# Optimization experiments

Hardware: AMD Instinct MI355X
Metric: run time of the kernel (lower is better)

Reference implementation:

```python
import jax, jax.numpy as jnp
import numpy as np


def setup_inputs() -> dict:
    key = jax.random.key(0)
    ks = jax.random.split(key, 5)
    B, G, p, C = 4, 3, 16, 768
    N = p * p
    s = 1.0 / np.sqrt(C)
    return {
        "x": jax.random.normal(ks[0], (B, G, N, C), dtype=jnp.float32),
        "wq": jax.random.normal(ks[1], (C, C), dtype=jnp.float32) * s,
        "w_kv": jax.random.normal(ks[2], (2 * C, C), dtype=jnp.float32) * s,
        "proj_w": jax.random.normal(ks[3], (C, C), dtype=jnp.float32) * s,
        "proj_b": jnp.zeros((C,), dtype=jnp.float32),
    }


def reference(x, wq, w_kv, proj_w, proj_b):
    NUM_HEADS = 12
    B, G, N, C = x.shape  # G == 3 (triplane)
    p = int(round(N ** 0.5))
    H = NUM_HEADS
    D = C // H

    x5 = x.reshape(B, G, p, p, C)

    # Queries: for plane i, tokens in (row a, col b) order; block layout (i, b, n)
    q_x = jnp.transpose(x5, (1, 0, 2, 3, 4)).reshape(G, B, N, C)  # (3,B,N,C)

    # Context per token (a,b) of plane i: row a of plane (i+1)%3  ++  col b of plane (i+2)%3
    rows_src = jnp.stack([x5[:, (i + 1) % G] for i in range(G)], axis=0)  # (3,B,p,p,C)
    cols_src = jnp.stack([x5[:, (i + 2) % G] for i in range(G)], axis=0)  # (3,B,p,p,C)

    # row a broadcast over column index b -> (3,B,a,b,p,C)
    row_ctx = jnp.broadcast_to(rows_src[:, :, :, None, :, :], (G, B, p, p, p, C)).reshape(G, B, N, p, C)
    # column b broadcast over row index a -> (3,B,a,b,p,C)
    cols_t = jnp.transpose(cols_src, (0, 1, 3, 2, 4))  # (3,B,b,r,C)
    col_ctx = jnp.broadcast_to(cols_t[:, :, None, :, :, :], (G, B, p, p, p, C)).reshape(G, B, N, p, C)

    context = jnp.concatenate([row_ctx, col_ctx], axis=3)  # (3,B,N,2p,C)

    # Projections (torch Linear: y = x @ W^T, no bias for q/kv)
    q = (q_x @ wq.T).reshape(G, B, N, H, D)
    kv = context @ w_kv.T  # (3,B,N,2p,2C)
    k = kv[..., :C].reshape(G, B, N, 2 * p, H, D)
    v = kv[..., C:].reshape(G, B, N, 2 * p, H, D)

    scale = 1.0 / np.sqrt(D)
    scores = jnp.einsum("gbnhd,gbnkhd->gbnhk", q, k) * scale
    attn = jax.nn.softmax(scores, axis=-1)
    out = jnp.einsum("gbnhk,gbnkhd->gbnhd", attn, v).reshape(G, B, N, C)

    # Faithful to original: flat (i,b,n) block order reinterpreted as (B,3,N,C)
    out = out.reshape(B, G, N, C)
    out = out @ proj_w.T + proj_b
    return out
```

## Files before the change

### kernel.cpp

```cpp
#include <hip/hip_runtime.h>
#include <hip/hip_bf16.h>

#define Bc 4
#define Gc 3
#define Nc 256
#define Cc_ 768
#define Dc 64
#define Mrows (Bc*Gc*Nc)
#define QKVc (3*Cc_)
#define Koff Cc_
#define Voff (2*Cc_)

typedef _Float16 half_t;
typedef __attribute__((ext_vector_type(8))) _Float16 f16x8;
typedef __attribute__((ext_vector_type(4))) float f32x4;

#define XN   (Mrows*Cc_)
#define WQN  (Cc_*Cc_)
#define WKVN (2*Cc_*Cc_)
#define PWN  (Cc_*Cc_)

__global__ __launch_bounds__(256) void cvt_all(
    const float* __restrict__ x, const float* __restrict__ wq,
    const float* __restrict__ wkv, const float* __restrict__ pw,
    half_t* __restrict__ x16, half_t* __restrict__ wq16,
    half_t* __restrict__ wkv16, half_t* __restrict__ pw16)
{
    const size_t e = ((size_t)blockIdx.x * 256 + threadIdx.x) * 8;
    const float* s; half_t* d;
    if (e < XN)                    { s = x   + e;                     d = x16   + e; }
    else if (e < XN + WQN)         { s = wq  + (e - XN);              d = wq16  + (e - XN); }
    else if (e < XN + WQN + WKVN)  { s = wkv + (e - XN - WQN);        d = wkv16 + (e - XN - WQN); }
    else                           { s = pw  + (e - XN - WQN - WKVN); d = pw16  + (e - XN - WQN - WKVN); }
    const float4 a = *(const float4*)s;
    const float4 b = *(const float4*)(s + 4);
    f16x8 o;
    o[0] = (half_t)a.x; o[1] = (half_t)a.y; o[2] = (half_t)a.z; o[3] = (half_t)a.w;
    o[4] = (half_t)b.x; o[5] = (half_t)b.y; o[6] = (half_t)b.z; o[7] = (half_t)b.w;
    *(f16x8*)d = o;
}

template<typename OutT, bool BIAS>
__global__ __launch_bounds__(256) void gemm16(
    const half_t* __restrict__ A, const half_t* __restrict__ W,
    OutT* __restrict__ C, const float* __restrict__ bias,
    int M, int Nn, int K)
{
    __shared__ __attribute__((aligned(16))) half_t sm[3][2][4][128][8];

    const int tid = threadIdx.x;
    const int w   = tid >> 6;
    const int l   = tid & 63;
    const int wm  = w >> 1;
    const int wn  = w & 1;
    const int m0  = blockIdx.y << 7;
    const int n0  = blockIdx.x << 7;

    f32x4 acc[4][4] = {};

    auto stage = [&](int buf, int k0) {
        #pragma unroll
        for (int i = 0; i < 2; ++i) {
            const int c   = w * 2 + i;
            const int kg  = c >> 1;
            const int r0  = (c & 1) * 64;
            const half_t* ga = A + (size_t)(m0 + r0 + l) * K + k0 + kg * 8;
            const half_t* gb = W + (size_t)(n0 + r0 + l) * K + k0 + kg * 8;
            __builtin_amdgcn_global_load_lds(
                (__attribute__((address_space(1))) void*)ga,
                (__attribute__((address_space(3))) void*)&sm[buf][0][kg][r0][0],
                16, 0, 0);
            __builtin_amdgcn_global_load_lds(
                (__attribute__((address_space(1))) void*)gb,
                (__attribute__((address_space(3))) void*)&sm[buf][1][kg][r0][0],
                16, 0, 0);
        }
    };

    const int NT = K >> 5;
    stage(0, 0);
    stage(1, 32);

    const int kg = l >> 4;
    const int lr = l & 15;
    int cur = 0;

    for (int t = 0; t < NT; ++t) {
        if (t + 1 < NT) asm volatile("s_waitcnt vmcnt(4)" ::: "memory");
        else            asm volatile("s_waitcnt vmcnt(0)" ::: "memory");
        __builtin_amdgcn_s_barrier();
        if (t + 2 < NT) {
            int nb = cur + 2; if (nb >= 3) nb -= 3;
            stage(nb, (t + 2) << 5);
        }

        f16x8 af[4], bf[4];
        #pragma unroll
        for (int mi = 0; mi < 4; ++mi)
            af[mi] = *(const f16x8*)&sm[cur][0][kg][wm * 64 + mi * 16 + lr][0];
        #pragma unroll
        for (int ni = 0; ni < 4; ++ni)
            bf[ni] = *(const f16x8*)&sm[cur][1][kg][wn * 64 + ni * 16 + lr][0];

        #pragma unroll
        for (int mi = 0; mi < 4; ++mi)
            #pragma unroll
            for (int ni = 0; ni < 4; ++ni)
                acc[mi][ni] = __builtin_amdgcn_mfma_f32_16x16x32_f16(
                    af[mi], bf[ni], acc[mi][ni], 0, 0, 0);

        cur = (cur == 2) ? 0 : cur + 1;
    }

    const int lq = l >> 4;
    #pragma unroll
    for (int ni = 0; ni < 4; ++ni) {
        const int gcol = n0 + wn * 64 + ni * 16 + lr;
        const float bv = BIAS ? bias[gcol] : 0.f;
        #pragma unroll
        for (int mi = 0; mi < 4; ++mi) {
            const int grow = m0 + wm * 64 + mi * 16 + lq * 4;
            #pragma unroll
            for (int r = 0; r < 4; ++r)
                C[(size_t)(grow + r) * Nn + gcol] = (OutT)(acc[mi][ni][r] + bv);
        }
    }
}

__global__ __launch_bounds__(256) void attn_kernel(
    const half_t* __restrict__ QKV,
    half_t* __restrict__ Oa)
{
    const int t  = blockIdx.x;
    const int g  = t >> 10;
    const int b  = (t >> 8) & 3;
    const int n  = t & 255;
    const int a  = n >> 4;
    const int bc = n & 15;

    __shared__ float qs[Cc_];
    __shared__ int   rows[32];

    const int qrow = (b * Gc + g) * Nc + n;
    if (threadIdx.x < 96) {
        const f16x8 v = ((const f16x8*)(QKV + (size_t)qrow * QKVc))[threadIdx.x];
        #pragma unroll
        for (int jj = 0; jj < 8; ++jj) qs[threadIdx.x * 8 + jj] = (float)v[jj];
    }
    if (threadIdx.x < 32) {
        const int j = threadIdx.x;
        int g1 = g + 1; if (g1 >= 3) g1 -= 3;
        int g2 = g + 2; if (g2 >= 3) g2 -= 3;
        rows[j] = (j < 16) ? ((b * Gc + g1) * Nc + a * 16 + j)
                           : ((b * Gc + g2) * Nc + (j - 16) * 16 + bc);
    }
    __syncthreads();

    const int wave = threadIdx.x >> 6;
    const int lane = threadIdx.x & 63;
    const int j    = lane & 31;
    const int dh   = lane >> 5;
    const size_t kvrow = (size_t)rows[j] * QKVc;

    for (int hh = 0; hh < 3; ++hh) {
        const int h = wave + hh * 4;
        const f16x8* kp = (const f16x8*)(QKV + kvrow + Koff + h * Dc + dh * 32);
        const float* qp = qs + h * Dc + dh * 32;
        float s = 0.f;
        #pragma unroll
        for (int c = 0; c < 4; ++c) {
            const f16x8 k8 = kp[c];
            #pragma unroll
            for (int e = 0; e < 8; ++e) s = fmaf(qp[c * 8 + e], (float)k8[e], s);
        }
        s += __shfl_xor(s, 32);
        s *= 0.125f;

        float m = s;
        #pragma unroll
        for (int off = 16; off >= 1; off >>= 1) m = fmaxf(m, __shfl_xor(m, off));
        const float e = __expf(s - m);
        float lsum = e;
        #pragma unroll
        for (int off = 16; off >= 1; off >>= 1) lsum += __shfl_xor(lsum, off);
        const float pr = e / lsum;

        float o = 0.f;
        #pragma unroll 8
        for (int jj = 0; jj < 32; ++jj) {
            const float pj = __shfl(pr, jj);
            o = fmaf(pj, (float)QKV[(size_t)rows[jj] * QKVc + Voff + h * Dc + lane], o);
        }
        Oa[(size_t)t * Cc_ + h * Dc + lane] = (half_t)o;
    }
}

extern "C" void kernel_launch(void* const* d_in, const int* in_sizes, int n_in,
                              void* d_out, int out_size, void* d_ws, size_t ws_size,
                              hipStream_t stream) {
    const float* x   = (const float*)d_in[0];
    const float* wq  = (const float*)d_in[1];
    const float* wkv = (const float*)d_in[2];
    const float* pw  = (const float*)d_in[3];
    const float* pb  = (const float*)d_in[4];
    float* out = (float*)d_out;

    half_t* x16   = (half_t*)d_ws;
    half_t* w3    = x16 + XN;
    half_t* pw16  = w3 + WQN + WKVN;
    half_t* QKV16 = pw16 + PWN;
    half_t* ATT16 = QKV16 + (size_t)Mrows * QKVc;

    const dim3 blk(256);

    cvt_all<<<dim3((XN + WQN + WKVN + PWN) / 8 / 256), blk, 0, stream>>>(
        x, wq, wkv, pw, x16, w3, w3 + WQN, pw16);

    gemm16<half_t, false><<<dim3(QKVc / 128, Mrows / 128), blk, 0, stream>>>(
        x16, w3, QKV16, nullptr, Mrows, QKVc, Cc_);

    attn_kernel<<<dim3(Mrows), blk, 0, stream>>>(QKV16, ATT16);

    gemm16<float, true><<<dim3(Cc_ / 128, Mrows / 128), blk, 0, stream>>>(
        ATT16, pw16, out, pb, Mrows, Cc_, Cc_);
}
```

Baseline: 85.54 us.

## Fuse fp32-to-fp16 conversion into GEMM loads and drop separate convert kernel

Removes the standalone conversion kernel and has the GEMMs read fp32 inputs and weights directly. The conversion to fp16 happens in registers before the shared-memory write. The load pipeline changes from async global-to-LDS triple buffering to register-staged double buffering. The wq and w_kv weights are selected per block via a split pointer, so no concatenated weight copy is needed. This saves one launch and a full write and re-read of the fp16 copies. In exchange, the GEMMs read twice the bytes, weights are converted again in every block that uses them, and the register-staged pipeline may overlap memory and compute less well.

```diff
diff --git a/kernel.cpp b/kernel.cpp
--- a/kernel.cpp
+++ b/kernel.cpp
@@ -15,38 +15,22 @@
 typedef __attribute__((ext_vector_type(8))) _Float16 f16x8;
 typedef __attribute__((ext_vector_type(4))) float f32x4;
 
-#define XN   (Mrows*Cc_)
-#define WQN  (Cc_*Cc_)
-#define WKVN (2*Cc_*Cc_)
-#define PWN  (Cc_*Cc_)
-
-__global__ __launch_bounds__(256) void cvt_all(
-    const float* __restrict__ x, const float* __restrict__ wq,
-    const float* __restrict__ wkv, const float* __restrict__ pw,
-    half_t* __restrict__ x16, half_t* __restrict__ wq16,
-    half_t* __restrict__ wkv16, half_t* __restrict__ pw16)
-{
-    const size_t e = ((size_t)blockIdx.x * 256 + threadIdx.x) * 8;
-    const float* s; half_t* d;
-    if (e < XN)                    { s = x   + e;                     d = x16   + e; }
-    else if (e < XN + WQN)         { s = wq  + (e - XN);              d = wq16  + (e - XN); }
-    else if (e < XN + WQN + WKVN)  { s = wkv + (e - XN - WQN);        d = wkv16 + (e - XN - WQN); }
-    else                           { s = pw  + (e - XN - WQN - WKVN); d = pw16  + (e - XN - WQN - WKVN); }
-    const float4 a = *(const float4*)s;
-    const float4 b = *(const float4*)(s + 4);
+__device__ inline f16x8 cv8(const float4& x, const float4& y) {
     f16x8 o;
-    o[0] = (half_t)a.x; o[1] = (half_t)a.y; o[2] = (half_t)a.z; o[3] = (half_t)a.w;
-    o[4] = (half_t)b.x; o[5] = (half_t)b.y; o[6] = (half_t)b.z; o[7] = (half_t)b.w;
-    *(f16x8*)d = o;
-}
-
-template<typename OutT, bool BIAS>
+    o[0] = (half_t)x.x; o[1] = (half_t)x.y; o[2] = (half_t)x.z; o[3] = (half_t)x.w;
+    o[4] = (half_t)y.x; o[5] = (half_t)y.y; o[6] = (half_t)y.z; o[7] = (half_t)y.w;
+    return o;
+}
+
+template<bool A_F32, bool W_F32, typename OutT, bool BIAS>
 __global__ __launch_bounds__(256) void gemm16(
-    const half_t* __restrict__ A, const half_t* __restrict__ W,
+    const void* __restrict__ Av, const void* __restrict__ W1v,
+    const void* __restrict__ W2v, int wsplit,
     OutT* __restrict__ C, const float* __restrict__ bias,
     int M, int Nn, int K)
 {
-    __shared__ __attribute__((aligned(16))) half_t sm[3][2][4][128][8];
+    __shared__ __attribute__((aligned(16))) half_t smA[2][4][128][8];
+    __shared__ __attribute__((aligned(16))) half_t smB[2][4][128][8];
 
     const int tid = threadIdx.x;
     const int w   = tid >> 6;
@@ -56,51 +40,68 @@
     const int m0  = blockIdx.y << 7;
     const int n0  = blockIdx.x << 7;
 
+    const void* Wv; int nrow0;
+    if (n0 < wsplit) { Wv = W1v; nrow0 = n0; }
+    else             { Wv = W2v; nrow0 = n0 - wsplit; }
+
+    const int srow = tid & 127;
+    const int skg0 = (tid >> 7) << 1;
+
+    float4 raf[2][2], rbf[2][2];
+    f16x8  rah[2],    rbh[2];
+
+    auto gload = [&](int k0) {
+        #pragma unroll
+        for (int q = 0; q < 2; ++q) {
+            const int kg = skg0 + q;
+            const size_t ia = (size_t)(m0 + srow) * K + k0 + kg * 8;
+            const size_t ib = (size_t)(nrow0 + srow) * K + k0 + kg * 8;
+            if constexpr (A_F32) {
+                const float* p = (const float*)Av + ia;
+                raf[q][0] = *(const float4*)p; raf[q][1] = *(const float4*)(p + 4);
+            } else {
+                rah[q] = *(const f16x8*)((const half_t*)Av + ia);
+            }
+            if constexpr (W_F32) {
+                const float* p = (const float*)Wv + ib;
+                rbf[q][0] = *(const float4*)p; rbf[q][1] = *(const float4*)(p + 4);
+            } else {
+                rbh[q] = *(const f16x8*)((const half_t*)Wv + ib);
+            }
+        }
+    };
+    auto swrite = [&](int buf) {
+        #pragma unroll
+        for (int q = 0; q < 2; ++q) {
+            const int kg = skg0 + q;
+            f16x8 oa, ob;
+            if constexpr (A_F32) oa = cv8(raf[q][0], raf[q][1]); else oa = rah[q];
+            if constexpr (W_F32) ob = cv8(rbf[q][0], rbf[q][1]); else ob = rbh[q];
+            *(f16x8*)&smA[buf][kg][srow][0] = oa;
+            *(f16x8*)&smB[buf][kg][srow][0] = ob;
+        }
+    };
+
     f32x4 acc[4][4] = {};
 
-    auto stage = [&](int buf, int k0) {
-        #pragma unroll
-        for (int i = 0; i < 2; ++i) {
-            const int c   = w * 2 + i;
-            const int kg  = c >> 1;
-            const int r0  = (c & 1) * 64;
-            const half_t* ga = A + (size_t)(m0 + r0 + l) * K + k0 + kg * 8;
-            const half_t* gb = W + (size_t)(n0 + r0 + l) * K + k0 + kg * 8;
-            __builtin_amdgcn_global_load_lds(
-                (__attribute__((address_space(1))) void*)ga,
-                (__attribute__((address_space(3))) void*)&sm[buf][0][kg][r0][0],
-                16, 0, 0);
-            __builtin_amdgcn_global_load_lds(
-                (__attribute__((address_space(1))) void*)gb,
-                (__attribute__((address_space(3))) void*)&sm[buf][1][kg][r0][0],
-                16, 0, 0);
-        }
-    };
-
     const int NT = K >> 5;
-    stage(0, 0);
-    stage(1, 32);
+    gload(0);  swrite(0);
+    gload(32);
 
     const int kg = l >> 4;
     const int lr = l & 15;
     int cur = 0;
 
     for (int t = 0; t < NT; ++t) {
-        if (t + 1 < NT) asm volatile("s_waitcnt vmcnt(4)" ::: "memory");
-        else            asm volatile("s_waitcnt vmcnt(0)" ::: "memory");
-        __builtin_amdgcn_s_barrier();
-        if (t + 2 < NT) {
-            int nb = cur + 2; if (nb >= 3) nb -= 3;
-            stage(nb, (t + 2) << 5);
-        }
+        __syncthreads();
 
         f16x8 af[4], bf[4];
         #pragma unroll
         for (int mi = 0; mi < 4; ++mi)
-            af[mi] = *(const f16x8*)&sm[cur][0][kg][wm * 64 + mi * 16 + lr][0];
+            af[mi] = *(const f16x8*)&smA[cur][kg][wm * 64 + mi * 16 + lr][0];
         #pragma unroll
         for (int ni = 0; ni < 4; ++ni)
-            bf[ni] = *(const f16x8*)&sm[cur][1][kg][wn * 64 + ni * 16 + lr][0];
+            bf[ni] = *(const f16x8*)&smB[cur][kg][wn * 64 + ni * 16 + lr][0];
 
         #pragma unroll
         for (int mi = 0; mi < 4; ++mi)
@@ -109,7 +110,11 @@
                 acc[mi][ni] = __builtin_amdgcn_mfma_f32_16x16x32_f16(
                     af[mi], bf[ni], acc[mi][ni], 0, 0, 0);
 
-        cur = (cur == 2) ? 0 : cur + 1;
+        if (t + 1 < NT) {
+            swrite(cur ^ 1);
+            if (t + 2 < NT) gload((t + 2) << 5);
+        }
+        cur ^= 1;
     }
 
     const int lq = l >> 4;
@@ -205,22 +210,18 @@
     const float* pb  = (const float*)d_in[4];
     float* out = (float*)d_out;
 
-    half_t* x16   = (half_t*)d_ws;
-    half_t* w3    = x16 + XN;
-    half_t* pw16  = w3 + WQN + WKVN;
-    half_t* QKV16 = pw16 + PWN;
+    half_t* QKV16 = (half_t*)d_ws;
     half_t* ATT16 = QKV16 + (size_t)Mrows * QKVc;
 
     const dim3 blk(256);
 
-    cvt_all<<<dim3((XN + WQN + WKVN + PWN) / 8 / 256), blk, 0, stream>>>(
-        x, wq, wkv, pw, x16, w3, w3 + WQN, pw16);
-
-    gemm16<half_t, false><<<dim3(QKVc / 128, Mrows / 128), blk, 0, stream>>>(
-        x16, w3, QKV16, nullptr, Mrows, QKVc, Cc_);
+    gemm16<true, true, half_t, false>
+        <<<dim3(QKVc / 128, Mrows / 128), blk, 0, stream>>>(
+        x, wq, wkv, Cc_, QKV16, nullptr, Mrows, QKVc, Cc_);
 
     attn_kernel<<<dim3(Mrows), blk, 0, stream>>>(QKV16, ATT16);
 
-    gemm16<float, true><<<dim3(Cc_ / 128, Mrows / 128), blk, 0, stream>>>(
-        ATT16, pw16, out, pb, Mrows, Cc_, Cc_);
-}
+    gemm16<false, true, float, true>
+        <<<dim3(Cc_ / 128, Mrows / 128), blk, 0, stream>>>(
+        ATT16, pw, pw, Cc_, out, pb, Mrows, Cc_, Cc_);
+}
```

Result: slower. 120.0 us (+40.3%).

## Fuse all stages into one persistent cooperative kernel with grid syncs

Applied to the files above, without the earlier changes.

Replaces the four separate launches (convert, QKV GEMM, attention, projection GEMM) with a single cooperative kernel of 256 persistent blocks that loops over the work of each stage, with grid-wide syncs between stages. The aim is to cut launch overhead and inter-kernel gaps. In exchange, each stage now runs on only 256 blocks: the QKV GEMM has 432 tiles and attention has 3072 tokens, so blocks loop several times. Occupancy may also drop because the shared-memory union is sized for the largest stage. The original multi-kernel path is kept as a fallback if the cooperative launch fails.

```diff
diff --git a/kernel.cpp b/kernel.cpp
--- a/kernel.cpp
+++ b/kernel.cpp
@@ -1,5 +1,8 @@
 #include <hip/hip_runtime.h>
 #include <hip/hip_bf16.h>
+#include <hip/hip_cooperative_groups.h>
+
+namespace cg = cooperative_groups;
 
 #define Bc 4
 #define Gc 3
@@ -19,42 +22,38 @@
 #define WQN  (Cc_*Cc_)
 #define WKVN (2*Cc_*Cc_)
 #define PWN  (Cc_*Cc_)
-
-__global__ __launch_bounds__(256) void cvt_all(
-    const float* __restrict__ x, const float* __restrict__ wq,
-    const float* __restrict__ wkv, const float* __restrict__ pw,
-    half_t* __restrict__ x16, half_t* __restrict__ wq16,
-    half_t* __restrict__ wkv16, half_t* __restrict__ pw16)
-{
-    const size_t e = ((size_t)blockIdx.x * 256 + threadIdx.x) * 8;
-    const float* s; half_t* d;
-    if (e < XN)                    { s = x   + e;                     d = x16   + e; }
-    else if (e < XN + WQN)         { s = wq  + (e - XN);              d = wq16  + (e - XN); }
-    else if (e < XN + WQN + WKVN)  { s = wkv + (e - XN - WQN);        d = wkv16 + (e - XN - WQN); }
-    else                           { s = pw  + (e - XN - WQN - WKVN); d = pw16  + (e - XN - WQN - WKVN); }
-    const float4 a = *(const float4*)s;
-    const float4 b = *(const float4*)(s + 4);
+#define CVTN ((XN+WQN+WKVN+PWN)/8)
+
+#define QKV_TILES ((QKVc/128)*(Mrows/128))
+#define PRJ_TILES ((Cc_/128)*(Mrows/128))
+
+#define GRID_BLKS 256
+
+__device__ __forceinline__ f16x8 cv8(const float4& x, const float4& y) {
     f16x8 o;
-    o[0] = (half_t)a.x; o[1] = (half_t)a.y; o[2] = (half_t)a.z; o[3] = (half_t)a.w;
-    o[4] = (half_t)b.x; o[5] = (half_t)b.y; o[6] = (half_t)b.z; o[7] = (half_t)b.w;
-    *(f16x8*)d = o;
-}
+    o[0] = (half_t)x.x; o[1] = (half_t)x.y; o[2] = (half_t)x.z; o[3] = (half_t)x.w;
+    o[4] = (half_t)y.x; o[5] = (half_t)y.y; o[6] = (half_t)y.z; o[7] = (half_t)y.w;
+    return o;
+}
+
+union ShMem {
+    struct { half_t sm[3][2][4][128][8]; } g;
+    struct { float qs[Cc_]; int rows[32]; } a;
+};
 
 template<typename OutT, bool BIAS>
-__global__ __launch_bounds__(256) void gemm16(
+__device__ __forceinline__ void gemm_tile(
+    ShMem& shm,
     const half_t* __restrict__ A, const half_t* __restrict__ W,
     OutT* __restrict__ C, const float* __restrict__ bias,
-    int M, int Nn, int K)
-{
-    __shared__ __attribute__((aligned(16))) half_t sm[3][2][4][128][8];
-
+    int m0, int n0, int Nn, int K)
+{
+    auto& sm = shm.g.sm;
     const int tid = threadIdx.x;
     const int w   = tid >> 6;
     const int l   = tid & 63;
     const int wm  = w >> 1;
     const int wn  = w & 1;
-    const int m0  = blockIdx.y << 7;
-    const int n0  = blockIdx.x << 7;
 
     f32x4 acc[4][4] = {};
 
@@ -127,19 +126,17 @@
     }
 }
 
-__global__ __launch_bounds__(256) void attn_kernel(
-    const half_t* __restrict__ QKV,
-    half_t* __restrict__ Oa)
-{
-    const int t  = blockIdx.x;
+__device__ __forceinline__ void attn_token(
+    ShMem& shm, const half_t* __restrict__ QKV, half_t* __restrict__ Oa, int t)
+{
+    float* qs   = shm.a.qs;
+    int*   rows = shm.a.rows;
+
     const int g  = t >> 10;
     const int b  = (t >> 8) & 3;
     const int n  = t & 255;
     const int a  = n >> 4;
     const int bc = n & 15;
-
-    __shared__ float qs[Cc_];
-    __shared__ int   rows[32];
 
     const int qrow = (b * Gc + g) * Nc + n;
     if (threadIdx.x < 96) {
@@ -193,6 +190,97 @@
         }
         Oa[(size_t)t * Cc_ + h * Dc + lane] = (half_t)o;
     }
+    __syncthreads();
+}
+
+__device__ __forceinline__ void cvt_chunk(
+    size_t e, const float* __restrict__ x, const float* __restrict__ wq,
+    const float* __restrict__ wkv, const float* __restrict__ pw,
+    half_t* __restrict__ x16, half_t* __restrict__ w3,
+    half_t* __restrict__ pw16)
+{
+    const float* s; half_t* d;
+    if (e < XN)                    { s = x   + e;                     d = x16  + e; }
+    else if (e < XN + WQN)         { s = wq  + (e - XN);              d = w3   + (e - XN); }
+    else if (e < XN + WQN + WKVN)  { s = wkv + (e - XN - WQN);        d = w3 + WQN + (e - XN - WQN); }
+    else                           { s = pw  + (e - XN - WQN - WKVN); d = pw16 + (e - XN - WQN - WKVN); }
+    const float4 a4 = *(const float4*)s;
+    const float4 b4 = *(const float4*)(s + 4);
+    *(f16x8*)d = cv8(a4, b4);
+}
+
+__global__ __launch_bounds__(256) void fused_all(
+    const float* __restrict__ x,  const float* __restrict__ wq,
+    const float* __restrict__ wkv, const float* __restrict__ pw,
+    const float* __restrict__ pb, float* __restrict__ out,
+    half_t* __restrict__ ws)
+{
+    __shared__ ShMem shm;
+
+    half_t* x16   = ws;
+    half_t* w3    = x16 + XN;
+    half_t* pw16  = w3 + WQN + WKVN;
+    half_t* QKV16 = pw16 + PWN;
+    half_t* ATT16 = QKV16 + (size_t)Mrows * QKVc;
+
+    const int nb  = gridDim.x;
+    const int bid = blockIdx.x;
+
+    for (size_t v = (size_t)bid * 256 + threadIdx.x; v < CVTN; v += (size_t)nb * 256)
+        cvt_chunk(v * 8, x, wq, wkv, pw, x16, w3, pw16);
+
+    cg::this_grid().sync();
+
+    for (int tile = bid; tile < QKV_TILES; tile += nb) {
+        const int bx = tile % (QKVc / 128);
+        const int by = tile / (QKVc / 128);
+        gemm_tile<half_t, false>(shm, x16, w3, QKV16, nullptr,
+                                 by * 128, bx * 128, QKVc, Cc_);
+        __syncthreads();
+    }
+
+    cg::this_grid().sync();
+
+    for (int t = bid; t < Mrows; t += nb)
+        attn_token(shm, QKV16, ATT16, t);
+
+    cg::this_grid().sync();
+
+    for (int tile = bid; tile < PRJ_TILES; tile += nb) {
+        const int bx = tile % (Cc_ / 128);
+        const int by = tile / (Cc_ / 128);
+        gemm_tile<float, true>(shm, ATT16, pw16, out, pb,
+                               by * 128, bx * 128, Cc_, Cc_);
+        __syncthreads();
+    }
+}
+
+__global__ __launch_bounds__(256) void cvt_all(
+    const float* __restrict__ x, const float* __restrict__ wq,
+    const float* __restrict__ wkv, const float* __restrict__ pw,
+    half_t* __restrict__ x16, half_t* __restrict__ w3,
+    half_t* __restrict__ pw16)
+{
+    cvt_chunk(((size_t)blockIdx.x * 256 + threadIdx.x) * 8,
+              x, wq, wkv, pw, x16, w3, pw16);
+}
+
+template<typename OutT, bool BIAS>
+__global__ __launch_bounds__(256) void gemm16(
+    const half_t* __restrict__ A, const half_t* __restrict__ W,
+    OutT* __restrict__ C, const float* __restrict__ bias,
+    int M, int Nn, int K)
+{
+    __shared__ ShMem shm;
+    gemm_tile<OutT, BIAS>(shm, A, W, C, bias,
+                          blockIdx.y << 7, blockIdx.x << 7, Nn, K);
+}
+
+__global__ __launch_bounds__(256) void attn_kernel(
+    const half_t* __restrict__ QKV, half_t* __restrict__ Oa)
+{
+    __shared__ ShMem shm;
+    attn_token(shm, QKV, Oa, blockIdx.x);
 }
 
 extern "C" void kernel_launch(void* const* d_in, const int* in_sizes, int n_in,
@@ -204,23 +292,26 @@
     const float* pw  = (const float*)d_in[3];
     const float* pb  = (const float*)d_in[4];
     float* out = (float*)d_out;
-
-    half_t* x16   = (half_t*)d_ws;
-    half_t* w3    = x16 + XN;
-    half_t* pw16  = w3 + WQN + WKVN;
-    half_t* QKV16 = pw16 + PWN;
-    half_t* ATT16 = QKV16 + (size_t)Mrows * QKVc;
-
-    const dim3 blk(256);
-
-    cvt_all<<<dim3((XN + WQN + WKVN + PWN) / 8 / 256), blk, 0, stream>>>(
-        x, wq, wkv, pw, x16, w3, w3 + WQN, pw16);
-
-    gemm16<half_t, false><<<dim3(QKVc / 128, Mrows / 128), blk, 0, stream>>>(
-        x16, w3, QKV16, nullptr, Mrows, QKVc, Cc_);
-
-    attn_kernel<<<dim3(Mrows), blk, 0, stream>>>(QKV16, ATT16);
-
-    gemm16<float, true><<<dim3(Cc_ / 128, Mrows / 128), blk, 0, stream>>>(
-        ATT16, pw16, out, pb, Mrows, Cc_, Cc_);
-}
+    half_t* ws = (half_t*)d_ws;
+
+    void* args[] = { (void*)&x, (void*)&wq, (void*)&wkv, (void*)&pw,
+                     (void*)&pb, (void*)&out, (void*)&ws };
+    hipError_t rc = hipLaunchCooperativeKernel(
+        (const void*)fused_all, dim3(GRID_BLKS), dim3(256), args, 0, stream);
+
+    if (rc != hipSuccess) {
+        half_t* x16   = ws;
+        half_t* w3    = x16 + XN;
+        half_t* pw16  = w3 + WQN + WKVN;
+        half_t* QKV16 = pw16 + PWN;
+        half_t* ATT16 = QKV16 + (size_t)Mrows * QKVc;
+        const dim3 blk(256);
+        cvt_all<<<dim3(CVTN / 256), blk, 0, stream>>>(
+            x, wq, wkv, pw, x16, w3, pw16);
+        gemm16<half_t, false><<<dim3(QKVc / 128, Mrows / 128), blk, 0, stream>>>(
+            x16, w3, QKV16, nullptr, Mrows, QKVc, Cc_);
+        attn_kernel<<<dim3(Mrows), blk, 0, stream>>>(QKV16, ATT16);
+        gemm16<float, true><<<dim3(Cc_ / 128, Mrows / 128), blk, 0, stream>>>(
+            ATT16, pw16, out, pb, Mrows, Cc_, Cc_);
+    }
+}
```

Measured after the change: 244.5 us. 186% more time.
